# Optimization experiments

Measured on AMD Instinct MI355X. Metric: run time of the kernel, lower is better.

Reference implementation:

```python
import jax, jax.numpy as jnp
import numpy as np

EMBED_DIM = 1024


def setup_inputs() -> dict:
    key = jax.random.key(0)
    ks = jax.random.split(key, 9)
    d = EMBED_DIM
    s = 1.0 / np.sqrt(d)
    x = jax.random.normal(ks[0], (4, 4096, d), dtype=jnp.float32)
    Wq = jax.random.normal(ks[1], (d, d), dtype=jnp.float32) * s
    bq = jax.random.normal(ks[2], (d,), dtype=jnp.float32) * 0.01
    Wk = jax.random.normal(ks[3], (d, d), dtype=jnp.float32) * s
    bk = jax.random.normal(ks[4], (d,), dtype=jnp.float32) * 0.01
    Wv = jax.random.normal(ks[5], (d, d), dtype=jnp.float32) * s
    bv = jax.random.normal(ks[6], (d,), dtype=jnp.float32) * 0.01
    Wo = jax.random.normal(ks[7], (d, d), dtype=jnp.float32) * s
    bo = jax.random.normal(ks[8], (d,), dtype=jnp.float32) * 0.01
    return {"x": x, "Wq": Wq, "bq": bq, "Wk": Wk, "bk": bk,
            "Wv": Wv, "bv": bv, "Wo": Wo, "bo": bo}


def reference(x, Wq, bq, Wk, bk, Wv, bv, Wo, bo):
    # x: [b, s, d]; single-head attention, scale = 1/sqrt(d)
    b, s, d = x.shape
    q = x @ Wq + bq
    k = x @ Wk + bk
    v = x @ Wv + bv
    scale = 1.0 / jnp.sqrt(jnp.asarray(d, x.dtype))
    scores = jnp.einsum('bqd,bkd->bqk', q, k) * scale  # [b, s, s]
    causal = jnp.tril(jnp.ones((s, s), dtype=bool))
    scores = jnp.where(causal, scores, jnp.asarray(-jnp.inf, scores.dtype))
    attn = jax.nn.softmax(scores, axis=-1)
    ctx = jnp.einsum('bqk,bkd->bqd', attn, v)
    return ctx @ Wo + bo
```

## Files before the change

### kernel.cpp

```cpp
#include <hip/hip_runtime.h>


typedef unsigned short u16;
typedef __attribute__((ext_vector_type(4))) unsigned short u16x4;
typedef __attribute__((ext_vector_type(8))) unsigned short u16x8;
typedef __attribute__((ext_vector_type(8))) __bf16 bf16x8;
typedef __attribute__((ext_vector_type(4))) float f32x4;

typedef const __attribute__((address_space(1))) void* as1cp;
typedef __attribute__((address_space(3))) void* as3p;

struct GemmPtrs {
  const u16* A[4];
  const u16* B[4];
  const float* bias[4];
  void* C[4];
};
struct TransPtrs {
  const void* in[4];
  u16* out[4];
};
struct SmPtrs {
  u16* P[4];
};

__device__ __forceinline__ u16 f2bf(float f) {
  union { float f; unsigned int i; } c; c.f = f;
  unsigned int r = c.i + 0x7fffu + ((c.i >> 16) & 1u);
  return (u16)(r >> 16);
}
__device__ __forceinline__ float bf2f(u16 u) {
  union { unsigned int i; float f; } c; c.i = ((unsigned int)u) << 16;
  return c.f;
}

__global__ __launch_bounds__(256) void cast_f32_bf16(const float* __restrict__ in,
                                                     u16* __restrict__ out, int n4) {
  int i = blockIdx.x * blockDim.x + threadIdx.x;
  if (i >= n4) return;
  float4 v = ((const float4*)in)[i];
  u16x4 u;
  u.x = f2bf(v.x); u.y = f2bf(v.y); u.z = f2bf(v.z); u.w = f2bf(v.w);
  ((u16x4*)out)[i] = u;
}

template <bool IN_F32>
__global__ __launch_bounds__(256) void transpose_to_bf16(TransPtrs tp, int R, int C) {
  __shared__ u16 t[32][34];
  int z = blockIdx.z;
  int tx = threadIdx.x, ty = threadIdx.y;
  int c0 = blockIdx.x * 32, r0 = blockIdx.y * 32;
#pragma unroll
  for (int dy = 0; dy < 4; ++dy) {
    int r = r0 + ty + dy * 8;
    int c = c0 + tx;
    u16 hv;
    if (IN_F32) hv = f2bf(((const float*)tp.in[z])[(size_t)r * C + c]);
    else        hv = ((const u16*)tp.in[z])[(size_t)r * C + c];
    t[ty + dy * 8][tx] = hv;
  }
  __syncthreads();
  u16* op = tp.out[z];
#pragma unroll
  for (int dy = 0; dy < 4; ++dy) {
    int a = ty + dy * 8;
    op[(size_t)(c0 + a) * R + r0 + tx] = t[tx][a];
  }
}

__global__ __launch_bounds__(256) void softmax_causal(SmPtrs sp) {
  int row = blockIdx.x;
  u16* P = sp.P[blockIdx.y];
  int tid = threadIdx.x;
  int lane = tid & 63, wv = tid >> 6;
  u16x8* prow = (u16x8*)(P + (size_t)row * 4096);
  int nch = (row >> 3) + 1;
  int fend = ((row >> 7) + 1) << 4;
  int c0 = tid, c1 = tid + 256;
  bool a0 = c0 < nch, a1 = c1 < nch;
  float vals[16];
  float lmax = -3.0e38f;
  if (a0) {
    u16x8 u = prow[c0];
#pragma unroll
    for (int e = 0; e < 8; ++e) {
      float f = (c0 * 8 + e <= row) ? bf2f(u[e]) : -3.0e38f;
      vals[e] = f; lmax = fmaxf(lmax, f);
    }
  } else {
#pragma unroll
    for (int e = 0; e < 8; ++e) vals[e] = -3.0e38f;
  }
  if (a1) {
    u16x8 u = prow[c1];
#pragma unroll
    for (int e = 0; e < 8; ++e) {
      float f = (c1 * 8 + e <= row) ? bf2f(u[e]) : -3.0e38f;
      vals[8 + e] = f; lmax = fmaxf(lmax, f);
    }
  } else {
#pragma unroll
    for (int e = 0; e < 8; ++e) vals[8 + e] = -3.0e38f;
  }
  __shared__ float red[8];
#pragma unroll
  for (int off = 32; off > 0; off >>= 1) lmax = fmaxf(lmax, __shfl_down(lmax, off, 64));
  if (lane == 0) red[wv] = lmax;
  __syncthreads();
  float m2 = fmaxf(fmaxf(red[0], red[1]), fmaxf(red[2], red[3]));
  float lsum = 0.f;
#pragma unroll
  for (int e = 0; e < 16; ++e) {
    float ev = __expf(vals[e] - m2);
    vals[e] = ev;
    lsum += ev;
  }
#pragma unroll
  for (int off = 32; off > 0; off >>= 1) lsum += __shfl_down(lsum, off, 64);
  if (lane == 0) red[4 + wv] = lsum;
  __syncthreads();
  float inv = 1.0f / (red[4] + red[5] + red[6] + red[7]);
  if (a0) {
    u16x8 u;
#pragma unroll
    for (int e = 0; e < 8; ++e) u[e] = f2bf(vals[e] * inv);
    prow[c0] = u;
  }
  if (a1) {
    u16x8 u;
#pragma unroll
    for (int e = 0; e < 8; ++e) u[e] = f2bf(vals[8 + e] * inv);
    prow[c1] = u;
  }
  u16x8 zz = (u16x8)(u16)0;
  for (int c = nch + tid; c < fend; c += 256) prow[c] = zz;
}

template <int MODE, bool OUT_BF16, bool HAS_BIAS, int MAXSLOT, int KDIM, int LDB>
__global__ __launch_bounds__(256) void gemm_persist(GemmPtrs p, int N, float cscale) {
  __shared__ __align__(16) u16 As[2][128 * 64];
  __shared__ __align__(16) u16 Bs[2][128 * 64];
  int b = blockIdx.x;
  int x = b & 7, q = b >> 3;
  int tid = threadIdx.x, lane = tid & 63, wv = tid >> 6;
  int wm = (wv >> 1) * 64, wn = (wv & 1) * 64;
  int lrow = lane & 15, lquad = lane >> 4;
  int srow = lane >> 3, scol = ((lane & 7) ^ srow) * 8;

  struct TP { const u16* A; const u16* B; int niter, tm, tn, z; };
  auto tileOf = [&](int s) {
    TP t;
    if (MODE == 0) {
      int c = x + 8 * (s * 8 + (q >> 3));
      t.z = c >> 7;
      t.tm = (c & 127) << 7; t.tn = (q & 7) << 7; t.niter = KDIM >> 6;
    } else if (MODE == 1) {
      int c = x + 8 * (s * 8 + (q >> 3));
      int tt = c * 8 + (q & 7);
      t.z = tt / 528; int L = tt - t.z * 528;
      int i = (int)((__fsqrt_rn(8.f * (float)L + 1.f) - 1.f) * 0.5f);
      while ((i + 1) * (i + 2) / 2 <= L) ++i;
      while (i * (i + 1) / 2 > L) --i;
      t.tm = i << 7; t.tn = (L - ((i * (i + 1)) >> 1)) << 7; t.niter = KDIM >> 6;
    } else if (MODE == 2) {
      int w = q & 15, h = w >> 3;
      int i = (s == 0) ? (h ? 15 - x : x) : (h ? 16 + x : 31 - x);
      t.z = q >> 4; t.tm = i << 7; t.tn = (w & 7) << 7; t.niter = (i + 1) * 2;
    } else {
      int c = x + 8 * (s * 8 + (q >> 3));
      t.z = 0; t.tm = c << 7; t.tn = (q & 7) << 7; t.niter = KDIM >> 6;
    }
    t.A = p.A[t.z] + (size_t)t.tm * KDIM;
    t.B = p.B[t.z] + (size_t)t.tn * LDB;
    return t;
  };
  int nslot = (MODE == 1) ? ((q >> 3) == 0 ? 5 : 4) : MAXSLOT;
  int total = (MODE == 2) ? 66 : nslot * (KDIM >> 6);

  int aoff = (wv * 32 + srow) * KDIM + scol;
  int boff = (wv * 32 + srow) * LDB + scol;

  TP st = tileOf(0);
  int stk = 0, sslot = 0;
  const u16* gA = st.A + aoff;
  const u16* gB = st.B + boff;

  auto stageTo = [&](int sb) {
#pragma unroll
    for (int tt = 0; tt < 4; ++tt) {
      __builtin_amdgcn_global_load_lds((as1cp)(gA + tt * 8 * KDIM),
                                       (as3p)&As[sb][(wv * 4 + tt) * 512], 16, 0, 0);
      __builtin_amdgcn_global_load_lds((as1cp)(gB + tt * 8 * LDB),
                                       (as3p)&Bs[sb][(wv * 4 + tt) * 512], 16, 0, 0);
    }
  };
  auto adv = [&]() {
    gA += 64; gB += 64;
    if (++stk == st.niter) {
      stk = 0;
      if (++sslot < nslot) {
        st = tileOf(sslot);
        gA = st.A + aoff;
        gB = st.B + boff;
      }
    }
  };

  f32x4 acc[4][4];
#pragma unroll
  for (int i = 0; i < 4; ++i)
#pragma unroll
    for (int j = 0; j < 4; ++j) acc[i][j] = (f32x4){0.f, 0.f, 0.f, 0.f};

  auto compute = [&](int cb) __attribute__((always_inline)) {
#pragma unroll
    for (int ks = 0; ks < 64; ks += 32) {
      bf16x8 af[4], bg[4];
#pragma unroll
      for (int mt = 0; mt < 4; ++mt) {
        int r = wm + mt * 16 + lrow;
        int jb = (ks >> 3) + lquad;
        af[mt] = *(const bf16x8*)&As[cb][r * 64 + ((jb ^ (r & 7)) << 3)];
      }
#pragma unroll
      for (int nt = 0; nt < 4; ++nt) {
        int r = wn + nt * 16 + lrow;
        int jb = (ks >> 3) + lquad;
        bg[nt] = *(const bf16x8*)&Bs[cb][r * 64 + ((jb ^ (r & 7)) << 3)];
      }
#pragma unroll
      for (int mt = 0; mt < 4; ++mt)
#pragma unroll
        for (int nt = 0; nt < 4; ++nt)
          acc[mt][nt] = __builtin_amdgcn_mfma_f32_16x16x32_bf16(af[mt], bg[nt], acc[mt][nt], 0, 0, 0);
    }
  };

  TP ct = st;
  int cit = 0, cslot = 0;
  auto epi = [&]() {
    if (++cit == ct.niter) {
      const float* bias = HAS_BIAS ? p.bias[ct.z] : nullptr;
#pragma unroll
      for (int mt = 0; mt < 4; ++mt) {
#pragma unroll
        for (int reg = 0; reg < 4; ++reg) {
          int r = ct.tm + wm + mt * 16 + lquad * 4 + reg;
#pragma unroll
          for (int nt = 0; nt < 4; ++nt) {
            int cidx = ct.tn + wn + nt * 16 + lrow;
            float vvv = acc[mt][nt][reg] * cscale;
            if (HAS_BIAS) vvv += bias[cidx];
            if (OUT_BF16) ((u16*)p.C[ct.z])[(size_t)r * N + cidx] = f2bf(vvv);
            else          ((float*)p.C[ct.z])[(size_t)r * N + cidx] = vvv;
          }
        }
      }
#pragma unroll
      for (int i = 0; i < 4; ++i)
#pragma unroll
        for (int j = 0; j < 4; ++j) acc[i][j] = (f32x4){0.f, 0.f, 0.f, 0.f};
      cit = 0;
      if (++cslot < nslot) ct = tileOf(cslot);
    }
  };

  stageTo(0);
  adv();
  for (int it = 0; it < total; it += 2) {
    if (it + 1 < total) {
      stageTo(1);
      adv();
      asm volatile("s_waitcnt vmcnt(8)" ::: "memory");
    } else {
      asm volatile("s_waitcnt vmcnt(0)" ::: "memory");
    }
    asm volatile("s_barrier" ::: "memory");
    compute(0);
    asm volatile("s_barrier" ::: "memory");
    epi();
    if (it + 2 < total) {
      stageTo(0);
      adv();
      asm volatile("s_waitcnt vmcnt(8)" ::: "memory");
    } else {
      asm volatile("s_waitcnt vmcnt(0)" ::: "memory");
    }
    asm volatile("s_barrier" ::: "memory");
    compute(1);
    asm volatile("s_barrier" ::: "memory");
    epi();
  }
}

extern "C" void kernel_launch(void* const* d_in, const int* in_sizes, int n_in,
                              void* d_out, int out_size, void* d_ws, size_t ws_size,
                              hipStream_t stream) {
  const float* x  = (const float*)d_in[0];
  const float* Wq = (const float*)d_in[1];
  const float* bq = (const float*)d_in[2];
  const float* Wk = (const float*)d_in[3];
  const float* bk = (const float*)d_in[4];
  const float* Wv = (const float*)d_in[5];
  const float* bv = (const float*)d_in[6];
  const float* Wo = (const float*)d_in[7];
  const float* bo = (const float*)d_in[8];

  const int S = 4096, D = 1024;
  const size_t XE = (size_t)4 * S * D;
  const size_t BSE = (size_t)S * D;

  char* ws = (char*)d_ws;
  u16* xb  = (u16*)(ws + 0);
  u16* q   = (u16*)(ws + 33554432);
  u16* k   = (u16*)(ws + 67108864);
  u16* v   = (u16*)(ws + 100663296);
  u16* ctx = (u16*)(ws + 134217728);
  u16* wqT = (u16*)(ws + 167772160);
  u16* wkT = wqT + 1048576;
  u16* wvT = wkT + 1048576;
  u16* woT = wvT + 1048576;
  u16* attn2 = (u16*)(ws + 176160768);
  u16* attn0 = (u16*)d_out;
  u16* attn1 = attn0 + (size_t)S * S;
  u16* attn3 = v;
  u16* vT = xb;
  u16* attn[4] = {attn0, attn1, attn2, attn3};

  cast_f32_bf16<<<(int)(XE / 4 / 256), 256, 0, stream>>>(x, xb, (int)(XE / 4));
  {
    TransPtrs tp = {{Wq, Wk, Wv, Wo}, {wqT, wkT, wvT, woT}};
    transpose_to_bf16<true><<<dim3(32, 32, 4), dim3(32, 8), 0, stream>>>(tp, D, D);
  }
  {
    GemmPtrs gp = {{xb, xb, xb, xb}, {wqT, wkT, wvT, wqT},
                   {bq, bk, bv, bq}, {q, k, v, q}};
    gemm_persist<0, true, true, 6, 1024, 1024><<<512, 256, 0, stream>>>(gp, D, 1.0f);
  }
  {
    TransPtrs tp = {{v, v + BSE, v + 2 * BSE, v + 3 * BSE},
                    {vT, vT + BSE, vT + 2 * BSE, vT + 3 * BSE}};
    transpose_to_bf16<false><<<dim3(D / 32, S / 32, 4), dim3(32, 8), 0, stream>>>(tp, S, D);
  }
  {
    GemmPtrs gp = {{q, q + BSE, q + 2 * BSE, q + 3 * BSE},
                   {k, k + BSE, k + 2 * BSE, k + 3 * BSE},
                   {nullptr, nullptr, nullptr, nullptr},
                   {attn[0], attn[1], attn[2], attn[3]}};
    gemm_persist<1, true, false, 5, 1024, 1024><<<512, 256, 0, stream>>>(gp, S, 0.03125f);
  }
  {
    SmPtrs sp = {{attn[0], attn[1], attn[2], attn[3]}};
    softmax_causal<<<dim3(S, 4), 256, 0, stream>>>(sp);
  }
  {
    GemmPtrs gp = {{attn[0], attn[1], attn[2], attn[3]},
                   {vT, vT + BSE, vT + 2 * BSE, vT + 3 * BSE},
                   {nullptr, nullptr, nullptr, nullptr},
                   {ctx, ctx + BSE, ctx + 2 * BSE, ctx + 3 * BSE}};
    gemm_persist<2, true, false, 2, 4096, 4096><<<512, 256, 0, stream>>>(gp, D, 1.0f);
  }
  {
    GemmPtrs gp = {{ctx, ctx, ctx, ctx}, {woT, woT, woT, woT},
                   {bo, bo, bo, bo}, {d_out, d_out, d_out, d_out}};
    gemm_persist<3, false, true, 2, 1024, 1024><<<512, 256, 0, stream>>>(gp, D, 1.0f);
  }
}
```

Before: 512.2 us.

## Widen persistent GEMM tiles to 128x256 and halve the grid to 256 blocks

Grows each block's output tile from 128x128 to 128x256, doubling the B staging buffer and per-wave accumulators (4x8 MFMA tiles). The tile schedules for all four GEMM modes are remapped to the new tile shape, including a new triangular index for the causal QK^T. The grid drops to 256 persistent blocks, one per CU. The aim is more MFMA work per LDS load and less A re-fetch. In exchange it raises register and LDS pressure (launch_bounds 256,1), lowers occupancy, and gives coarser load balance on the causal modes.

Measured after the change: 626.4 us. +22.3%, slower.

```diff
diff --git a/kernel.cpp b/kernel.cpp
--- a/kernel.cpp
+++ b/kernel.cpp
@@ -137,13 +137,13 @@
 }
 
 template <int MODE, bool OUT_BF16, bool HAS_BIAS, int MAXSLOT, int KDIM, int LDB>
-__global__ __launch_bounds__(256) void gemm_persist(GemmPtrs p, int N, float cscale) {
+__global__ __launch_bounds__(256, 1) void gemm_persist(GemmPtrs p, int N, float cscale) {
   __shared__ __align__(16) u16 As[2][128 * 64];
-  __shared__ __align__(16) u16 Bs[2][128 * 64];
+  __shared__ __align__(16) u16 Bs[2][256 * 64];
   int b = blockIdx.x;
   int x = b & 7, q = b >> 3;
   int tid = threadIdx.x, lane = tid & 63, wv = tid >> 6;
-  int wm = (wv >> 1) * 64, wn = (wv & 1) * 64;
+  int wm = (wv >> 1) * 64, wn = (wv & 1) * 128;
   int lrow = lane & 15, lquad = lane >> 4;
   int srow = lane >> 3, scol = ((lane & 7) ^ srow) * 8;
 
@@ -151,34 +151,37 @@
   auto tileOf = [&](int s) {
     TP t;
     if (MODE == 0) {
-      int c = x + 8 * (s * 8 + (q >> 3));
-      t.z = c >> 7;
-      t.tm = (c & 127) << 7; t.tn = (q & 7) << 7; t.niter = KDIM >> 6;
+      int idx = s * 32 + q;
+      int ml = idx / 12, r = idx - ml * 12;
+      t.z = r >> 2;
+      t.tm = (ml * 8 + x) << 7; t.tn = (r & 3) << 8; t.niter = KDIM >> 6;
     } else if (MODE == 1) {
-      int c = x + 8 * (s * 8 + (q >> 3));
-      int tt = c * 8 + (q & 7);
-      t.z = tt / 528; int L = tt - t.z * 528;
-      int i = (int)((__fsqrt_rn(8.f * (float)L + 1.f) - 1.f) * 0.5f);
-      while ((i + 1) * (i + 2) / 2 <= L) ++i;
-      while (i * (i + 1) / 2 > L) --i;
-      t.tm = i << 7; t.tn = (L - ((i * (i + 1)) >> 1)) << 7; t.niter = KDIM >> 6;
+      int T = x * 136 + s * 32 + q;
+      t.z = T / 272; int L = T - t.z * 272;
+      int m = (int)(2.f * __fsqrt_rn((float)L + 1.f)) - 1;
+      if (m < 0) m = 0;
+      while ((( (m+1)*(m+1) + 2*(m+1) + ((m+1)&1) ) >> 2) <= L) ++m;
+      while ((( m*m + 2*m + (m&1) ) >> 2) > L) --m;
+      t.tm = m << 7; t.tn = (L - ((m*m + 2*m + (m&1)) >> 2)) << 8;
+      t.niter = KDIM >> 6;
     } else if (MODE == 2) {
-      int w = q & 15, h = w >> 3;
+      int w = q & 7, h = w >> 2;
       int i = (s == 0) ? (h ? 15 - x : x) : (h ? 16 + x : 31 - x);
-      t.z = q >> 4; t.tm = i << 7; t.tn = (w & 7) << 7; t.niter = (i + 1) * 2;
+      t.z = q >> 3; t.tm = i << 7; t.tn = (w & 3) << 8; t.niter = (i + 1) * 2;
     } else {
-      int c = x + 8 * (s * 8 + (q >> 3));
-      t.z = 0; t.tm = c << 7; t.tn = (q & 7) << 7; t.niter = KDIM >> 6;
+      int idx = s * 32 + q;
+      t.z = 0; t.tm = ((idx >> 2) * 8 + x) << 7; t.tn = (idx & 3) << 8;
+      t.niter = KDIM >> 6;
     }
     t.A = p.A[t.z] + (size_t)t.tm * KDIM;
     t.B = p.B[t.z] + (size_t)t.tn * LDB;
     return t;
   };
-  int nslot = (MODE == 1) ? ((q >> 3) == 0 ? 5 : 4) : MAXSLOT;
+  int nslot = (MODE == 1) ? (q < 8 ? 5 : 4) : MAXSLOT;
   int total = (MODE == 2) ? 66 : nslot * (KDIM >> 6);
 
   int aoff = (wv * 32 + srow) * KDIM + scol;
-  int boff = (wv * 32 + srow) * LDB + scol;
+  int boff = (wv * 64 + srow) * LDB + scol;
 
   TP st = tileOf(0);
   int stk = 0, sslot = 0;
@@ -187,12 +190,13 @@
 
   auto stageTo = [&](int sb) {
 #pragma unroll
-    for (int tt = 0; tt < 4; ++tt) {
+    for (int tt = 0; tt < 4; ++tt)
       __builtin_amdgcn_global_load_lds((as1cp)(gA + tt * 8 * KDIM),
                                        (as3p)&As[sb][(wv * 4 + tt) * 512], 16, 0, 0);
+#pragma unroll
+    for (int tt = 0; tt < 8; ++tt)
       __builtin_amdgcn_global_load_lds((as1cp)(gB + tt * 8 * LDB),
-                                       (as3p)&Bs[sb][(wv * 4 + tt) * 512], 16, 0, 0);
-    }
+                                       (as3p)&Bs[sb][(wv * 8 + tt) * 512], 16, 0, 0);
   };
   auto adv = [&]() {
     gA += 64; gB += 64;
@@ -206,16 +210,16 @@
     }
   };
 
-  f32x4 acc[4][4];
+  f32x4 acc[4][8];
 #pragma unroll
   for (int i = 0; i < 4; ++i)
 #pragma unroll
-    for (int j = 0; j < 4; ++j) acc[i][j] = (f32x4){0.f, 0.f, 0.f, 0.f};
+    for (int j = 0; j < 8; ++j) acc[i][j] = (f32x4){0.f, 0.f, 0.f, 0.f};
 
   auto compute = [&](int cb) __attribute__((always_inline)) {
 #pragma unroll
     for (int ks = 0; ks < 64; ks += 32) {
-      bf16x8 af[4], bg[4];
+      bf16x8 af[4], bg[8];
 #pragma unroll
       for (int mt = 0; mt < 4; ++mt) {
         int r = wm + mt * 16 + lrow;
@@ -223,7 +227,7 @@
         af[mt] = *(const bf16x8*)&As[cb][r * 64 + ((jb ^ (r & 7)) << 3)];
       }
 #pragma unroll
-      for (int nt = 0; nt < 4; ++nt) {
+      for (int nt = 0; nt < 8; ++nt) {
         int r = wn + nt * 16 + lrow;
         int jb = (ks >> 3) + lquad;
         bg[nt] = *(const bf16x8*)&Bs[cb][r * 64 + ((jb ^ (r & 7)) << 3)];
@@ -231,7 +235,7 @@
 #pragma unroll
       for (int mt = 0; mt < 4; ++mt)
 #pragma unroll
-        for (int nt = 0; nt < 4; ++nt)
+        for (int nt = 0; nt < 8; ++nt)
           acc[mt][nt] = __builtin_amdgcn_mfma_f32_16x16x32_bf16(af[mt], bg[nt], acc[mt][nt], 0, 0, 0);
     }
   };
@@ -247,7 +251,7 @@
         for (int reg = 0; reg < 4; ++reg) {
           int r = ct.tm + wm + mt * 16 + lquad * 4 + reg;
 #pragma unroll
-          for (int nt = 0; nt < 4; ++nt) {
+          for (int nt = 0; nt < 8; ++nt) {
             int cidx = ct.tn + wn + nt * 16 + lrow;
             float vvv = acc[mt][nt][reg] * cscale;
             if (HAS_BIAS) vvv += bias[cidx];
@@ -259,7 +263,7 @@
 #pragma unroll
       for (int i = 0; i < 4; ++i)
 #pragma unroll
-        for (int j = 0; j < 4; ++j) acc[i][j] = (f32x4){0.f, 0.f, 0.f, 0.f};
+        for (int j = 0; j < 8; ++j) acc[i][j] = (f32x4){0.f, 0.f, 0.f, 0.f};
       cit = 0;
       if (++cslot < nslot) ct = tileOf(cslot);
     }
@@ -271,7 +275,7 @@
     if (it + 1 < total) {
       stageTo(1);
       adv();
-      asm volatile("s_waitcnt vmcnt(8)" ::: "memory");
+      asm volatile("s_waitcnt vmcnt(12)" ::: "memory");
     } else {
       asm volatile("s_waitcnt vmcnt(0)" ::: "memory");
     }
@@ -282,7 +286,7 @@
     if (it + 2 < total) {
       stageTo(0);
       adv();
-      asm volatile("s_waitcnt vmcnt(8)" ::: "memory");
+      asm volatile("s_waitcnt vmcnt(12)" ::: "memory");
     } else {
       asm volatile("s_waitcnt vmcnt(0)" ::: "memory");
     }
@@ -335,7 +339,7 @@
   {
     GemmPtrs gp = {{xb, xb, xb, xb}, {wqT, wkT, wvT, wqT},
                    {bq, bk, bv, bq}, {q, k, v, q}};
-    gemm_persist<0, true, true, 6, 1024, 1024><<<512, 256, 0, stream>>>(gp, D, 1.0f);
+    gemm_persist<0, true, true, 6, 1024, 1024><<<256, 256, 0, stream>>>(gp, D, 1.0f);
   }
   {
     TransPtrs tp = {{v, v + BSE, v + 2 * BSE, v + 3 * BSE},
@@ -347,7 +351,7 @@
                    {k, k + BSE, k + 2 * BSE, k + 3 * BSE},
                    {nullptr, nullptr, nullptr, nullptr},
                    {attn[0], attn[1], attn[2], attn[3]}};
-    gemm_persist<1, true, false, 5, 1024, 1024><<<512, 256, 0, stream>>>(gp, S, 0.03125f);
+    gemm_persist<1, true, false, 5, 1024, 1024><<<256, 256, 0, stream>>>(gp, S, 0.03125f);
   }
   {
     SmPtrs sp = {{attn[0], attn[1], attn[2], attn[3]}};
@@ -358,11 +362,11 @@
                    {vT, vT + BSE, vT + 2 * BSE, vT + 3 * BSE},
                    {nullptr, nullptr, nullptr, nullptr},
                    {ctx, ctx + BSE, ctx + 2 * BSE, ctx + 3 * BSE}};
-    gemm_persist<2, true, false, 2, 4096, 4096><<<512, 256, 0, stream>>>(gp, D, 1.0f);
+    gemm_persist<2, true, false, 2, 4096, 4096><<<256, 256, 0, stream>>>(gp, D, 1.0f);
   }
   {
     GemmPtrs gp = {{ctx, ctx, ctx, ctx}, {woT, woT, woT, woT},
                    {bo, bo, bo, bo}, {d_out, d_out, d_out, d_out}};
-    gemm_persist<3, false, true, 2, 1024, 1024><<<512, 256, 0, stream>>>(gp, D, 1.0f);
-  }
-}
+    gemm_persist<3, false, true, 2, 1024, 1024><<<256, 256, 0, stream>>>(gp, D, 1.0f);
+  }
+}
```
